# Performance work log

Measured on AMD Instinct MI355X. Metric: run time of the kernel, lower is better.

The kernel has to match this reference:

```python
import jax, jax.numpy as jnp
import numpy as np

TEMPERATURE = 0.07

def l2norm(x, eps=1e-12):
    # torch.nn.functional.normalize(dim=1): x / max(||x||, eps)
    n = jnp.sqrt(jnp.sum(x * x, axis=1, keepdims=True))
    return x / jnp.maximum(n, eps)

def setup_inputs() -> dict:
    key = jax.random.key(0)
    ks = jax.random.split(key, 8)
    B, D_in, H, M, Q, NNEG = 1024, 2048, 1024, 256, 65536, 16384
    return {
        "y1": jax.random.normal(ks[0], (B, D_in), dtype=jnp.float32),
        "y2": jax.random.normal(ks[1], (B, D_in), dtype=jnp.float32),
        "W_enc_q": jax.random.normal(ks[2], (D_in, H), dtype=jnp.float32) * 0.02,
        "W_enc_k": jax.random.normal(ks[3], (D_in, H), dtype=jnp.float32) * 0.02,
        "W_proj": jax.random.normal(ks[4], (H, M), dtype=jnp.float32) * 0.02,
        "queue": jax.random.normal(ks[5], (Q, M), dtype=jnp.float32),
        "sample_idx": jax.random.randint(ks[6], (NNEG,), 0, Q, dtype=jnp.int32),
        "write_idx": jnp.arange(B, dtype=jnp.int32),
    }

def reference(y1, y2, W_enc_q, W_enc_k, W_proj, queue, sample_idx, write_idx):
    # query path (trainable)
    q = l2norm((y2 @ W_enc_q) @ W_proj)                 # [B, M]
    # key path (no_grad in original)
    k = jax.lax.stop_gradient(l2norm((y1 @ W_enc_k) @ W_proj))  # [B, M]
    # sample negatives from GPU-resident queue (gather) + normalize
    neg = l2norm(queue[sample_idx])                     # [NNEG, M]
    pos_logits = jnp.sum(q * k, axis=1, keepdims=True)  # [B, 1]
    neg_logits = q @ neg.T                              # [B, NNEG]
    logits = jnp.concatenate([pos_logits, neg_logits], axis=1) / TEMPERATURE
    # cross_entropy with labels == 0
    loss = -jnp.mean(jax.nn.log_softmax(logits, axis=-1)[:, 0])
    # FIFO append modeled as circular-buffer scatter write
    new_queue = queue.at[write_idx].set(k)
    return loss, new_queue
```

## Files before the change

kernel.cpp:

```cpp
#include <hip/hip_runtime.h>
#include <hip/hip_bf16.h>
#include <math.h>
#include <stdint.h>


typedef __attribute__((ext_vector_type(4))) float floatx4;
typedef __attribute__((ext_vector_type(8))) short bf16x8;
typedef __attribute__((ext_vector_type(8))) unsigned short ushort8;

__device__ __forceinline__ unsigned short f2bf(float x) {
    union { float f; unsigned int u; } v; v.f = x;
    unsigned int r = v.u + 0x7FFFu + ((v.u >> 16) & 1u);
    return (unsigned short)(r >> 16);
}

__device__ __forceinline__ void async_cp16(const void* g, void* l) {
    auto gp = reinterpret_cast<const __attribute__((address_space(1))) unsigned int*>(
        reinterpret_cast<uintptr_t>(g));
    auto lp = reinterpret_cast<__attribute__((address_space(3))) unsigned int*>(
        reinterpret_cast<uintptr_t>(l));
    __builtin_amdgcn_global_load_lds(gp, lp, 16, 0, 0);
}

__global__ __launch_bounds__(256) void prep_all(
    const float* __restrict__ y2, const float* __restrict__ y1,
    const float* __restrict__ Wq, const float* __restrict__ Wk,
    const float* __restrict__ Wp,
    unsigned short* __restrict__ y2b, unsigned short* __restrict__ y1b,
    unsigned short* __restrict__ Wqb, unsigned short* __restrict__ Wkb,
    unsigned short* __restrict__ Wpt,
    int D, int H, int M) {
    __shared__ unsigned short tile[32][33];
    const int b = blockIdx.x, t = threadIdx.x;

    if (b < 4096) {
        const int g = b >> 10, i = b & 1023;
        const float* in = (g == 0) ? y2 : (g == 1) ? y1 : (g == 2) ? Wq : Wk;
        unsigned short* outp = (g == 0) ? y2b : (g == 1) ? y1b : (g == 2) ? Wqb : Wkb;
        long idx = (long)i * 256 + t;
        const float4* in4 = (const float4*)in;
        float4 a = in4[idx * 2], c = in4[idx * 2 + 1];
        ushort8 o;
        o[0] = f2bf(a.x); o[1] = f2bf(a.y); o[2] = f2bf(a.z); o[3] = f2bf(a.w);
        o[4] = f2bf(c.x); o[5] = f2bf(c.y); o[6] = f2bf(c.z); o[7] = f2bf(c.w);
        ((ushort8*)outp)[idx] = o;
        return;
    }
    int idx = b - 4096;
    const int R = H, C = M;
    int cb = C / 32;
    int c0 = (idx % cb) * 32, r0 = (idx / cb) * 32;
    int tx = t & 31, ty = t >> 5;
#pragma unroll
    for (int i = 0; i < 4; ++i)
        tile[ty + i * 8][tx] = f2bf(Wp[(size_t)(r0 + ty + i * 8) * C + c0 + tx]);
    __syncthreads();
#pragma unroll
    for (int i = 0; i < 4; ++i)
        Wpt[(size_t)(c0 + ty + i * 8) * R + r0 + tx] = tile[tx][ty + i * 8];
}

__global__ __launch_bounds__(256) void wc_plus(
    const unsigned short* __restrict__ Wpt,
    const unsigned short* __restrict__ Wqkb,
    unsigned short* __restrict__ Wct,
    const float* __restrict__ queue, const int* __restrict__ sidx,
    unsigned short* __restrict__ negb) {
    __shared__ unsigned short As[3][128 * 32];
    __shared__ unsigned short Bs[3][64 * 32];
    const int b = blockIdx.x, t = threadIdx.x;
    const int type = b % 3, id = b / 3;

    if (type == 0) {
        const int batch = id >> 6, rem = id & 63;
        const int row0 = (rem >> 5) * 128;
        const int col0 = (rem & 31) * 64;
        const unsigned short* A = Wpt;
        const unsigned short* Bp = Wqkb + (long)batch * 2048 * 1024;
        unsigned short* C = Wct + (long)batch * 256 * 2048;
        const int Ko = 1024, No = 2048, nIt = 32;
        const int lane = t & 63, wave = t >> 6;
        const int wr = wave >> 1, wc = wave & 1;
        const int lrow = lane & 15, quad = lane >> 4;

        floatx4 acc[4][2] = {};

        auto stage = [&](int kk, int p) {
            int c0 = t, c1 = t + 256;
            async_cp16(A + (size_t)(row0 + (c0 >> 2)) * Ko + kk + (c0 & 3) * 8,
                       (char*)(As[p]) + (size_t)c0 * 16);
            async_cp16(A + (size_t)(row0 + (c1 >> 2)) * Ko + kk + (c1 & 3) * 8,
                       (char*)(As[p]) + (size_t)c1 * 16);
            async_cp16(Bp + (size_t)(col0 + (t >> 2)) * Ko + kk + (t & 3) * 8,
                       (char*)(Bs[p]) + (size_t)t * 16);
        };
        auto compute = [&](int p) {
            bf16x8 af[4], bfr[2];
#pragma unroll
            for (int i = 0; i < 4; ++i)
                af[i] = *(const bf16x8*)(As[p] + (size_t)(wr * 64 + i * 16 + lrow) * 32 + quad * 8);
#pragma unroll
            for (int j = 0; j < 2; ++j)
                bfr[j] = *(const bf16x8*)(Bs[p] + (size_t)(wc * 32 + j * 16 + lrow) * 32 + quad * 8);
            __builtin_amdgcn_s_setprio(1);
#pragma unroll
            for (int i = 0; i < 4; ++i)
#pragma unroll
                for (int j = 0; j < 2; ++j)
                    acc[i][j] = __builtin_amdgcn_mfma_f32_16x16x32_bf16(af[i], bfr[j], acc[i][j], 0, 0, 0);
            __builtin_amdgcn_s_setprio(0);
        };

        stage(0, 0);
        stage(32, 1);
        for (int k = 0; k < nIt; ++k) {
            if (k + 2 < nIt) {
                stage((k + 2) * 32, (k + 2) % 3);
                asm volatile("s_waitcnt vmcnt(6)" ::: "memory");
            } else if (k + 2 == nIt) {
                asm volatile("s_waitcnt vmcnt(3)" ::: "memory");
            } else {
                asm volatile("s_waitcnt vmcnt(0)" ::: "memory");
            }
            __builtin_amdgcn_s_barrier();
            compute(k % 3);
            __builtin_amdgcn_s_barrier();
        }
#pragma unroll
        for (int i = 0; i < 4; ++i) {
            int grow = row0 + wr * 64 + i * 16 + quad * 4;
#pragma unroll
            for (int j = 0; j < 2; ++j) {
                int gcol = col0 + wc * 32 + j * 16 + lrow;
#pragma unroll
                for (int r = 0; r < 4; ++r)
                    C[(size_t)(grow + r) * No + gcol] = f2bf(acc[i][j][r]);
            }
        }
    } else {
        const int gid = id * 2 + (type == 2);
        const int w = t >> 6, lane = t & 63;
#pragma unroll
        for (int j = 0; j < 16; ++j) {
            int r = gid * 64 + w * 16 + j;
            const float4* src = (const float4*)(queue + (size_t)sidx[r] * 256);
            float4 v = src[lane];
            float ss = v.x * v.x + v.y * v.y + v.z * v.z + v.w * v.w;
#pragma unroll
            for (int off = 1; off < 64; off <<= 1) ss += __shfl_xor(ss, off);
            float inv = 1.f / fmaxf(sqrtf(ss), 1e-12f);
            unsigned short o[4] = { f2bf(v.x * inv), f2bf(v.y * inv),
                                    f2bf(v.z * inv), f2bf(v.w * inv) };
            *(unsigned long long*)(negb + (size_t)r * 256 + lane * 4) =
                *(unsigned long long*)o;
        }
    }
}

__global__ __launch_bounds__(256) void qk_plus(
    const unsigned short* __restrict__ Yb,
    const unsigned short* __restrict__ Wct,
    float* __restrict__ Pg,
    const float4* __restrict__ queue4, float4* __restrict__ newq4) {
    __shared__ unsigned short As[3][128 * 32];
    __shared__ unsigned short Bs[3][64 * 32];
    const int b = blockIdx.x, t = threadIdx.x;
    const int type = b % 3, id = b / 3;

    if (type == 0) {
        const int z = id >> 5, rem = id & 31;
        const int batch = z >> 2, split = z & 3;
        const int row0 = (rem >> 2) * 128;
        const int col0 = (rem & 3) * 64;
        const unsigned short* A = Yb + (long)batch * 1024 * 2048;
        const unsigned short* Bp = Wct + (long)batch * 256 * 2048;
        float* P = Pg + (long)z * 1024 * 256;
        const int Ko = 2048, No = 256, nIt = 16;
        const int kbeg = split * 512;
        const int lane = t & 63, wave = t >> 6;
        const int wr = wave >> 1, wc = wave & 1;
        const int lrow = lane & 15, quad = lane >> 4;

        floatx4 acc[4][2] = {};

        auto stage = [&](int kk, int p) {
            int c0 = t, c1 = t + 256;
            async_cp16(A + (size_t)(row0 + (c0 >> 2)) * Ko + kk + (c0 & 3) * 8,
                       (char*)(As[p]) + (size_t)c0 * 16);
            async_cp16(A + (size_t)(row0 + (c1 >> 2)) * Ko + kk + (c1 & 3) * 8,
                       (char*)(As[p]) + (size_t)c1 * 16);
            async_cp16(Bp + (size_t)(col0 + (t >> 2)) * Ko + kk + (t & 3) * 8,
                       (char*)(Bs[p]) + (size_t)t * 16);
        };
        auto compute = [&](int p) {
            bf16x8 af[4], bfr[2];
#pragma unroll
            for (int i = 0; i < 4; ++i)
                af[i] = *(const bf16x8*)(As[p] + (size_t)(wr * 64 + i * 16 + lrow) * 32 + quad * 8);
#pragma unroll
            for (int j = 0; j < 2; ++j)
                bfr[j] = *(const bf16x8*)(Bs[p] + (size_t)(wc * 32 + j * 16 + lrow) * 32 + quad * 8);
            __builtin_amdgcn_s_setprio(1);
#pragma unroll
            for (int i = 0; i < 4; ++i)
#pragma unroll
                for (int j = 0; j < 2; ++j)
                    acc[i][j] = __builtin_amdgcn_mfma_f32_16x16x32_bf16(af[i], bfr[j], acc[i][j], 0, 0, 0);
            __builtin_amdgcn_s_setprio(0);
        };

        stage(kbeg, 0);
        stage(kbeg + 32, 1);
        for (int k = 0; k < nIt; ++k) {
            if (k + 2 < nIt) {
                stage(kbeg + (k + 2) * 32, (k + 2) % 3);
                asm volatile("s_waitcnt vmcnt(6)" ::: "memory");
            } else if (k + 2 == nIt) {
                asm volatile("s_waitcnt vmcnt(3)" ::: "memory");
            } else {
                asm volatile("s_waitcnt vmcnt(0)" ::: "memory");
            }
            __builtin_amdgcn_s_barrier();
            compute(k % 3);
            __builtin_amdgcn_s_barrier();
        }
#pragma unroll
        for (int i = 0; i < 4; ++i) {
            int grow = row0 + wr * 64 + i * 16 + quad * 4;
#pragma unroll
            for (int j = 0; j < 2; ++j) {
                int gcol = col0 + wc * 32 + j * 16 + lrow;
#pragma unroll
                for (int r = 0; r < 4; ++r)
                    P[(size_t)(grow + r) * No + gcol] = acc[i][j][r];
            }
        }
    } else {
        const int cid = id * 2 + (type == 2);
        long base = (long)cid * 8192 + t;
#pragma unroll
        for (int o = 0; o < 4; ++o) {
            float4 v[8];
#pragma unroll
            for (int i = 0; i < 8; ++i) v[i] = queue4[base + (size_t)(o * 8 + i) * 256];
#pragma unroll
            for (int i = 0; i < 8; ++i) newq4[base + (size_t)(o * 8 + i) * 256] = v[i];
        }
    }
}

__global__ __launch_bounds__(256) void qk_finalize(const float* __restrict__ P,
                                                   const int* __restrict__ widx,
                                                   unsigned short* __restrict__ qkb,
                                                   float* __restrict__ newq,
                                                   float* __restrict__ pos,
                                                   float* __restrict__ sumexp,
                                                   int B_, int nsplit, float invT) {
    const int i = blockIdx.x, t = threadIdx.x;
    const long RM = (long)B_ * 256;
    float sq = 0.f, sk = 0.f;
    for (int s = 0; s < nsplit; ++s) {
        sq += P[(long)s * RM + (long)i * 256 + t];
        sk += P[(long)(nsplit + s) * RM + (long)i * 256 + t];
    }
    __shared__ float r0[256], r1[256], r2[256];
    r0[t] = sq * sq; r1[t] = sk * sk; r2[t] = sq * sk;
    __syncthreads();
    for (int off = 128; off > 0; off >>= 1) {
        if (t < off) { r0[t] += r0[t + off]; r1[t] += r1[t + off]; r2[t] += r2[t + off]; }
        __syncthreads();
    }
    float nq = fmaxf(sqrtf(r0[0]), 1e-12f);
    float nk = fmaxf(sqrtf(r1[0]), 1e-12f);
    float qn = sq / nq, kn = sk / nk;
    qkb[(size_t)i * 256 + t] = f2bf(qn);
    qkb[(size_t)(B_ + i) * 256 + t] = f2bf(kn);
    newq[(size_t)widx[i] * 256 + t] = kn;
    if (t == 0) {
        float p = (r2[0] / (nq * nk)) * invT;
        pos[i] = p;
        sumexp[i] = __expf(p);
    }
}

__global__ __launch_bounds__(256) void gemm_logits(const unsigned short* __restrict__ A,
                                                   const unsigned short* __restrict__ B,
                                                   float* __restrict__ sumexp,
                                                   int Ko, float invT) {
    __shared__ unsigned short As[128 * 64];
    __shared__ unsigned short Bs[128 * 64];
    __shared__ float rowred[128];
    const int row0 = blockIdx.y * 128, col0 = blockIdx.x * 128;
    const int t = threadIdx.x;
    const int lane = t & 63, wave = t >> 6;
    const int wr = wave >> 1, wc = wave & 1;
    const int lrow = lane & 15, quad = lane >> 4;

    floatx4 acc[4][4] = {};

    for (int kk = 0; kk < Ko; kk += 64) {
#pragma unroll
        for (int r = 0; r < 4; ++r) {
            int c = t + r * 256;
            async_cp16(A + (size_t)(row0 + (c >> 3)) * Ko + kk + (c & 7) * 8,
                       (char*)As + (size_t)c * 16);
            async_cp16(B + (size_t)(col0 + (c >> 3)) * Ko + kk + (c & 7) * 8,
                       (char*)Bs + (size_t)c * 16);
        }
        __syncthreads();
        bf16x8 af[4][2], bf[4][2];
#pragma unroll
        for (int i = 0; i < 4; ++i)
#pragma unroll
            for (int k2 = 0; k2 < 2; ++k2) {
                af[i][k2] = *(const bf16x8*)(As + (size_t)(wr * 64 + i * 16 + lrow) * 64 + k2 * 32 + quad * 8);
                bf[i][k2] = *(const bf16x8*)(Bs + (size_t)(wc * 64 + i * 16 + lrow) * 64 + k2 * 32 + quad * 8);
            }
#pragma unroll
        for (int k2 = 0; k2 < 2; ++k2)
#pragma unroll
            for (int i = 0; i < 4; ++i)
#pragma unroll
                for (int j = 0; j < 4; ++j)
                    acc[i][j] = __builtin_amdgcn_mfma_f32_16x16x32_bf16(af[i][k2], bf[j][k2], acc[i][j], 0, 0, 0);
        __syncthreads();
    }
    if (t < 128) rowred[t] = 0.f;
    __syncthreads();
#pragma unroll
    for (int i = 0; i < 4; ++i) {
#pragma unroll
        for (int r = 0; r < 4; ++r) {
            float s = 0.f;
#pragma unroll
            for (int j = 0; j < 4; ++j) s += __expf(acc[i][j][r] * invT);
            s += __shfl_xor(s, 1); s += __shfl_xor(s, 2);
            s += __shfl_xor(s, 4); s += __shfl_xor(s, 8);
            if (lrow == 0) atomicAdd(&rowred[wr * 64 + i * 16 + quad * 4 + r], s);
        }
    }
    __syncthreads();
    if (t < 128) atomicAdd(&sumexp[row0 + t], rowred[t]);
}

__global__ __launch_bounds__(256) void final_loss(const float* __restrict__ pos,
                                                  const float* __restrict__ sumexp,
                                                  float* __restrict__ out, int B_) {
    const int t = threadIdx.x;
    float acc = 0.f;
    for (int i = t; i < B_; i += 256) acc += logf(sumexp[i]) - pos[i];
    __shared__ float s[256];
    s[t] = acc;
    __syncthreads();
    for (int off = 128; off > 0; off >>= 1) {
        if (t < off) s[t] += s[t + off];
        __syncthreads();
    }
    if (t == 0) out[0] = s[0] / (float)B_;
}

extern "C" void kernel_launch(void* const* d_in, const int* in_sizes, int n_in,
                              void* d_out, int out_size, void* d_ws, size_t ws_size,
                              hipStream_t stream) {
    const float* y1    = (const float*)d_in[0];
    const float* y2    = (const float*)d_in[1];
    const float* Wq    = (const float*)d_in[2];
    const float* Wk    = (const float*)d_in[3];
    const float* Wp    = (const float*)d_in[4];
    const float* queue = (const float*)d_in[5];
    const int*   sidx  = (const int*)d_in[6];
    const int*   widx  = (const int*)d_in[7];
    float* out = (float*)d_out;

    const int B    = in_sizes[7];
    const int NNEG = in_sizes[6];
    const int D    = in_sizes[0] / B;
    const int H    = in_sizes[2] / D;
    const int M    = in_sizes[4] / H;
    const float invT = 1.0f / 0.07f;
    const int NS_P = 4;

    float* ws  = (float*)d_ws;
    float* Pp     = ws;
    float* pos    = Pp + (size_t)2 * NS_P * B * M;
    float* sumexp = pos + B;
    unsigned short* us = (unsigned short*)(sumexp + B);
    unsigned short* y2b  = us;
    unsigned short* y1b  = y2b + (size_t)B * D;
    unsigned short* Wqb  = y1b + (size_t)B * D;
    unsigned short* Wkb  = Wqb + (size_t)D * H;
    unsigned short* Wpt  = Wkb + (size_t)D * H;
    unsigned short* Wct  = Wpt + (size_t)M * H;
    unsigned short* qkb  = Wct + (size_t)2 * M * D;
    unsigned short* negb = qkb + (size_t)2 * B * M;

    const int nPrep = 4 * 1024 + (H / 32) * (M / 32);
    prep_all<<<nPrep, 256, 0, stream>>>(y2, y1, Wq, Wk, Wp,
                                        y2b, y1b, Wqb, Wkb, Wpt, D, H, M);

    wc_plus<<<384, 256, 0, stream>>>(Wpt, Wqb, Wct, queue, sidx, negb);

    qk_plus<<<768, 256, 0, stream>>>(y2b, Wct, Pp,
                                     (const float4*)queue, (float4*)(out + 1));

    qk_finalize<<<B, 256, 0, stream>>>(Pp, widx, qkb, out + 1, pos, sumexp,
                                       B, NS_P, invT);

    gemm_logits<<<dim3(NNEG / 128, B / 128), 256, 0, stream>>>(
        qkb, negb, sumexp, M, invT);

    final_loss<<<1, 256, 0, stream>>>(pos, sumexp, out, B);
}
```

Before: 216.6 us.

## Rebalance work across kernels and fuse final loss into logits GEMM

The negative-sample gather and normalize moves from wc_plus into prep_all, and the queue copy moves from qk_plus into wc_plus. The qk GEMM becomes a standalone kernel with 64-row tiles, giving 512 blocks instead of 256 GEMM blocks. The final_loss launch is removed: the last gemm_logits block to finish, found through an atomic counter that qk_finalize resets, computes the mean loss. This cuts one launch and rebalances co-scheduled work between stages, at the cost of a threadfence and atomic per block plus smaller GEMM tiles with less reuse.

```diff
diff --git a/kernel.cpp b/kernel.cpp
--- a/kernel.cpp
+++ b/kernel.cpp
@@ -29,6 +29,8 @@
     unsigned short* __restrict__ y2b, unsigned short* __restrict__ y1b,
     unsigned short* __restrict__ Wqb, unsigned short* __restrict__ Wkb,
     unsigned short* __restrict__ Wpt,
+    const float* __restrict__ queue, const int* __restrict__ sidx,
+    unsigned short* __restrict__ negb,
     int D, int H, int M) {
     __shared__ unsigned short tile[32][33];
     const int b = blockIdx.x, t = threadIdx.x;
@@ -46,30 +48,48 @@
         ((ushort8*)outp)[idx] = o;
         return;
     }
-    int idx = b - 4096;
-    const int R = H, C = M;
-    int cb = C / 32;
-    int c0 = (idx % cb) * 32, r0 = (idx / cb) * 32;
-    int tx = t & 31, ty = t >> 5;
-#pragma unroll
-    for (int i = 0; i < 4; ++i)
-        tile[ty + i * 8][tx] = f2bf(Wp[(size_t)(r0 + ty + i * 8) * C + c0 + tx]);
-    __syncthreads();
-#pragma unroll
-    for (int i = 0; i < 4; ++i)
-        Wpt[(size_t)(c0 + ty + i * 8) * R + r0 + tx] = tile[tx][ty + i * 8];
+    if (b < 4352) {
+        int idx = b - 4096;
+        const int R = H, C = M;
+        int cb = C / 32;
+        int c0 = (idx % cb) * 32, r0 = (idx / cb) * 32;
+        int tx = t & 31, ty = t >> 5;
+#pragma unroll
+        for (int i = 0; i < 4; ++i)
+            tile[ty + i * 8][tx] = f2bf(Wp[(size_t)(r0 + ty + i * 8) * C + c0 + tx]);
+        __syncthreads();
+#pragma unroll
+        for (int i = 0; i < 4; ++i)
+            Wpt[(size_t)(c0 + ty + i * 8) * R + r0 + tx] = tile[tx][ty + i * 8];
+        return;
+    }
+    const int gid = b - 4352;
+    const int w = t >> 6, lane = t & 63;
+#pragma unroll
+    for (int j = 0; j < 16; ++j) {
+        int r = gid * 64 + w * 16 + j;
+        const float4* src = (const float4*)(queue + (size_t)sidx[r] * 256);
+        float4 v = src[lane];
+        float ss = v.x * v.x + v.y * v.y + v.z * v.z + v.w * v.w;
+#pragma unroll
+        for (int off = 1; off < 64; off <<= 1) ss += __shfl_xor(ss, off);
+        float inv = 1.f / fmaxf(sqrtf(ss), 1e-12f);
+        unsigned short o[4] = { f2bf(v.x * inv), f2bf(v.y * inv),
+                                f2bf(v.z * inv), f2bf(v.w * inv) };
+        *(unsigned long long*)(negb + (size_t)r * 256 + lane * 4) =
+            *(unsigned long long*)o;
+    }
 }
 
 __global__ __launch_bounds__(256) void wc_plus(
     const unsigned short* __restrict__ Wpt,
     const unsigned short* __restrict__ Wqkb,
     unsigned short* __restrict__ Wct,
-    const float* __restrict__ queue, const int* __restrict__ sidx,
-    unsigned short* __restrict__ negb) {
+    const float4* __restrict__ queue4, float4* __restrict__ newq4) {
     __shared__ unsigned short As[3][128 * 32];
     __shared__ unsigned short Bs[3][64 * 32];
     const int b = blockIdx.x, t = threadIdx.x;
-    const int type = b % 3, id = b / 3;
+    const int type = b % 5, id = b / 5;
 
     if (type == 0) {
         const int batch = id >> 6, rem = id & 63;
@@ -138,113 +158,88 @@
             }
         }
     } else {
-        const int gid = id * 2 + (type == 2);
-        const int w = t >> 6, lane = t & 63;
-#pragma unroll
-        for (int j = 0; j < 16; ++j) {
-            int r = gid * 64 + w * 16 + j;
-            const float4* src = (const float4*)(queue + (size_t)sidx[r] * 256);
-            float4 v = src[lane];
-            float ss = v.x * v.x + v.y * v.y + v.z * v.z + v.w * v.w;
-#pragma unroll
-            for (int off = 1; off < 64; off <<= 1) ss += __shfl_xor(ss, off);
-            float inv = 1.f / fmaxf(sqrtf(ss), 1e-12f);
-            unsigned short o[4] = { f2bf(v.x * inv), f2bf(v.y * inv),
-                                    f2bf(v.z * inv), f2bf(v.w * inv) };
-            *(unsigned long long*)(negb + (size_t)r * 256 + lane * 4) =
-                *(unsigned long long*)o;
-        }
-    }
-}
-
-__global__ __launch_bounds__(256) void qk_plus(
+        const int cid = id * 4 + (type - 1);
+        long base = (long)cid * 8192 + t;
+#pragma unroll
+        for (int o = 0; o < 4; ++o) {
+            float4 v[8];
+#pragma unroll
+            for (int i = 0; i < 8; ++i) v[i] = queue4[base + (size_t)(o * 8 + i) * 256];
+#pragma unroll
+            for (int i = 0; i < 8; ++i) newq4[base + (size_t)(o * 8 + i) * 256] = v[i];
+        }
+    }
+}
+
+__global__ __launch_bounds__(256) void qk_gemm(
     const unsigned short* __restrict__ Yb,
     const unsigned short* __restrict__ Wct,
-    float* __restrict__ Pg,
-    const float4* __restrict__ queue4, float4* __restrict__ newq4) {
-    __shared__ unsigned short As[3][128 * 32];
+    float* __restrict__ Pg) {
+    __shared__ unsigned short As[3][64 * 32];
     __shared__ unsigned short Bs[3][64 * 32];
-    const int b = blockIdx.x, t = threadIdx.x;
-    const int type = b % 3, id = b / 3;
-
-    if (type == 0) {
-        const int z = id >> 5, rem = id & 31;
-        const int batch = z >> 2, split = z & 3;
-        const int row0 = (rem >> 2) * 128;
-        const int col0 = (rem & 3) * 64;
-        const unsigned short* A = Yb + (long)batch * 1024 * 2048;
-        const unsigned short* Bp = Wct + (long)batch * 256 * 2048;
-        float* P = Pg + (long)z * 1024 * 256;
-        const int Ko = 2048, No = 256, nIt = 16;
-        const int kbeg = split * 512;
-        const int lane = t & 63, wave = t >> 6;
-        const int wr = wave >> 1, wc = wave & 1;
-        const int lrow = lane & 15, quad = lane >> 4;
-
-        floatx4 acc[4][2] = {};
-
-        auto stage = [&](int kk, int p) {
-            int c0 = t, c1 = t + 256;
-            async_cp16(A + (size_t)(row0 + (c0 >> 2)) * Ko + kk + (c0 & 3) * 8,
-                       (char*)(As[p]) + (size_t)c0 * 16);
-            async_cp16(A + (size_t)(row0 + (c1 >> 2)) * Ko + kk + (c1 & 3) * 8,
-                       (char*)(As[p]) + (size_t)c1 * 16);
-            async_cp16(Bp + (size_t)(col0 + (t >> 2)) * Ko + kk + (t & 3) * 8,
-                       (char*)(Bs[p]) + (size_t)t * 16);
-        };
-        auto compute = [&](int p) {
-            bf16x8 af[4], bfr[2];
-#pragma unroll
-            for (int i = 0; i < 4; ++i)
-                af[i] = *(const bf16x8*)(As[p] + (size_t)(wr * 64 + i * 16 + lrow) * 32 + quad * 8);
+    const int id = blockIdx.x, t = threadIdx.x;
+    const int z = id >> 6, rem = id & 63;
+    const int batch = z >> 2, split = z & 3;
+    const int row0 = (rem >> 2) * 64;
+    const int col0 = (rem & 3) * 64;
+    const unsigned short* A = Yb + (long)batch * 1024 * 2048;
+    const unsigned short* Bp = Wct + (long)batch * 256 * 2048;
+    float* P = Pg + (long)z * 1024 * 256;
+    const int Ko = 2048, No = 256, nIt = 16;
+    const int kbeg = split * 512;
+    const int lane = t & 63, wave = t >> 6;
+    const int wr = wave >> 1, wc = wave & 1;
+    const int lrow = lane & 15, quad = lane >> 4;
+
+    floatx4 acc[2][2] = {};
+
+    auto stage = [&](int kk, int p) {
+        async_cp16(A + (size_t)(row0 + (t >> 2)) * Ko + kk + (t & 3) * 8,
+                   (char*)(As[p]) + (size_t)t * 16);
+        async_cp16(Bp + (size_t)(col0 + (t >> 2)) * Ko + kk + (t & 3) * 8,
+                   (char*)(Bs[p]) + (size_t)t * 16);
+    };
+    auto compute = [&](int p) {
+        bf16x8 af[2], bfr[2];
+#pragma unroll
+        for (int i = 0; i < 2; ++i)
+            af[i] = *(const bf16x8*)(As[p] + (size_t)(wr * 32 + i * 16 + lrow) * 32 + quad * 8);
+#pragma unroll
+        for (int j = 0; j < 2; ++j)
+            bfr[j] = *(const bf16x8*)(Bs[p] + (size_t)(wc * 32 + j * 16 + lrow) * 32 + quad * 8);
+        __builtin_amdgcn_s_setprio(1);
+#pragma unroll
+        for (int i = 0; i < 2; ++i)
 #pragma unroll
             for (int j = 0; j < 2; ++j)
-                bfr[j] = *(const bf16x8*)(Bs[p] + (size_t)(wc * 32 + j * 16 + lrow) * 32 + quad * 8);
-            __builtin_amdgcn_s_setprio(1);
-#pragma unroll
-            for (int i = 0; i < 4; ++i)
-#pragma unroll
-                for (int j = 0; j < 2; ++j)
-                    acc[i][j] = __builtin_amdgcn_mfma_f32_16x16x32_bf16(af[i], bfr[j], acc[i][j], 0, 0, 0);
-            __builtin_amdgcn_s_setprio(0);
-        };
-
-        stage(kbeg, 0);
-        stage(kbeg + 32, 1);
-        for (int k = 0; k < nIt; ++k) {
-            if (k + 2 < nIt) {
-                stage(kbeg + (k + 2) * 32, (k + 2) % 3);
-                asm volatile("s_waitcnt vmcnt(6)" ::: "memory");
-            } else if (k + 2 == nIt) {
-                asm volatile("s_waitcnt vmcnt(3)" ::: "memory");
-            } else {
-                asm volatile("s_waitcnt vmcnt(0)" ::: "memory");
-            }
-            __builtin_amdgcn_s_barrier();
-            compute(k % 3);
-            __builtin_amdgcn_s_barrier();
-        }
-#pragma unroll
-        for (int i = 0; i < 4; ++i) {
-            int grow = row0 + wr * 64 + i * 16 + quad * 4;
-#pragma unroll
-            for (int j = 0; j < 2; ++j) {
-                int gcol = col0 + wc * 32 + j * 16 + lrow;
-#pragma unroll
-                for (int r = 0; r < 4; ++r)
-                    P[(size_t)(grow + r) * No + gcol] = acc[i][j][r];
-            }
-        }
-    } else {
-        const int cid = id * 2 + (type == 2);
-        long base = (long)cid * 8192 + t;
-#pragma unroll
-        for (int o = 0; o < 4; ++o) {
-            float4 v[8];
-#pragma unroll
-            for (int i = 0; i < 8; ++i) v[i] = queue4[base + (size_t)(o * 8 + i) * 256];
-#pragma unroll
-            for (int i = 0; i < 8; ++i) newq4[base + (size_t)(o * 8 + i) * 256] = v[i];
+                acc[i][j] = __builtin_amdgcn_mfma_f32_16x16x32_bf16(af[i], bfr[j], acc[i][j], 0, 0, 0);
+        __builtin_amdgcn_s_setprio(0);
+    };
+
+    stage(kbeg, 0);
+    stage(kbeg + 32, 1);
+    for (int k = 0; k < nIt; ++k) {
+        if (k + 2 < nIt) {
+            stage(kbeg + (k + 2) * 32, (k + 2) % 3);
+            asm volatile("s_waitcnt vmcnt(4)" ::: "memory");
+        } else if (k + 2 == nIt) {
+            asm volatile("s_waitcnt vmcnt(2)" ::: "memory");
+        } else {
+            asm volatile("s_waitcnt vmcnt(0)" ::: "memory");
+        }
+        __builtin_amdgcn_s_barrier();
+        compute(k % 3);
+        __builtin_amdgcn_s_barrier();
+    }
+#pragma unroll
+    for (int i = 0; i < 2; ++i) {
+        int grow = row0 + wr * 32 + i * 16 + quad * 4;
+#pragma unroll
+        for (int j = 0; j < 2; ++j) {
+            int gcol = col0 + wc * 32 + j * 16 + lrow;
+#pragma unroll
+            for (int r = 0; r < 4; ++r)
+                P[(size_t)(grow + r) * No + gcol] = acc[i][j][r];
         }
     }
 }
@@ -255,8 +250,10 @@
                                                    float* __restrict__ newq,
                                                    float* __restrict__ pos,
                                                    float* __restrict__ sumexp,
+                                                   unsigned int* __restrict__ ctr,
                                                    int B_, int nsplit, float invT) {
     const int i = blockIdx.x, t = threadIdx.x;
+    if (i == 0 && t == 0) *ctr = 0u;
     const long RM = (long)B_ * 256;
     float sq = 0.f, sk = 0.f;
     for (int s = 0; s < nsplit; ++s) {
@@ -286,7 +283,11 @@
 __global__ __launch_bounds__(256) void gemm_logits(const unsigned short* __restrict__ A,
                                                    const unsigned short* __restrict__ B,
                                                    float* __restrict__ sumexp,
-                                                   int Ko, float invT) {
+                                                   const float* __restrict__ pos,
+                                                   float* __restrict__ out,
+                                                   unsigned int* __restrict__ ctr,
+                                                   int Ko, int B_, int nblocks,
+                                                   float invT) {
     __shared__ unsigned short As[128 * 64];
     __shared__ unsigned short Bs[128 * 64];
     __shared__ float rowred[128];
@@ -341,22 +342,25 @@
     }
     __syncthreads();
     if (t < 128) atomicAdd(&sumexp[row0 + t], rowred[t]);
-}
-
-__global__ __launch_bounds__(256) void final_loss(const float* __restrict__ pos,
-                                                  const float* __restrict__ sumexp,
-                                                  float* __restrict__ out, int B_) {
-    const int t = threadIdx.x;
-    float acc = 0.f;
-    for (int i = t; i < B_; i += 256) acc += logf(sumexp[i]) - pos[i];
-    __shared__ float s[256];
-    s[t] = acc;
+
+    __threadfence();
     __syncthreads();
-    for (int off = 128; off > 0; off >>= 1) {
-        if (t < off) s[t] += s[t + off];
+    __shared__ int lastdone;
+    if (t == 0) lastdone = (atomicAdd(ctr, 1u) == (unsigned)(nblocks - 1));
+    __syncthreads();
+    if (lastdone) {
+        float accl = 0.f;
+        for (int i = t; i < B_; i += 256)
+            accl += logf(atomicAdd(&sumexp[i], 0.0f)) - pos[i];
+        __shared__ float sred[256];
+        sred[t] = accl;
         __syncthreads();
-    }
-    if (t == 0) out[0] = s[0] / (float)B_;
+        for (int off = 128; off > 0; off >>= 1) {
+            if (t < off) sred[t] += sred[t + off];
+            __syncthreads();
+        }
+        if (t == 0) out[0] = sred[0] / (float)B_;
+    }
 }
 
 extern "C" void kernel_launch(void* const* d_in, const int* in_sizes, int n_in,
@@ -384,7 +388,8 @@
     float* Pp     = ws;
     float* pos    = Pp + (size_t)2 * NS_P * B * M;
     float* sumexp = pos + B;
-    unsigned short* us = (unsigned short*)(sumexp + B);
+    unsigned int* ctr = (unsigned int*)(sumexp + B);
+    unsigned short* us = (unsigned short*)(ctr + 64);
     unsigned short* y2b  = us;
     unsigned short* y1b  = y2b + (size_t)B * D;
     unsigned short* Wqb  = y1b + (size_t)B * D;
@@ -394,20 +399,20 @@
     unsigned short* qkb  = Wct + (size_t)2 * M * D;
     unsigned short* negb = qkb + (size_t)2 * B * M;
 
-    const int nPrep = 4 * 1024 + (H / 32) * (M / 32);
+    const int nPrep = 4 * 1024 + (H / 32) * (M / 32) + NNEG / 64;
     prep_all<<<nPrep, 256, 0, stream>>>(y2, y1, Wq, Wk, Wp,
-                                        y2b, y1b, Wqb, Wkb, Wpt, D, H, M);
-
-    wc_plus<<<384, 256, 0, stream>>>(Wpt, Wqb, Wct, queue, sidx, negb);
-
-    qk_plus<<<768, 256, 0, stream>>>(y2b, Wct, Pp,
+                                        y2b, y1b, Wqb, Wkb, Wpt,
+                                        queue, sidx, negb, D, H, M);
+
+    wc_plus<<<640, 256, 0, stream>>>(Wpt, Wqb, Wct,
                                      (const float4*)queue, (float4*)(out + 1));
 
+    qk_gemm<<<512, 256, 0, stream>>>(y2b, Wct, Pp);
+
     qk_finalize<<<B, 256, 0, stream>>>(Pp, widx, qkb, out + 1, pos, sumexp,
-                                       B, NS_P, invT);
-
+                                       ctr, B, NS_P, invT);
+
+    const int nLog = (NNEG / 128) * (B / 128);
     gemm_logits<<<dim3(NNEG / 128, B / 128), 256, 0, stream>>>(
-        qkb, negb, sumexp, M, invT);
-
-    final_loss<<<1, 256, 0, stream>>>(pos, sumexp, out, B);
-}
+        qkb, negb, sumexp, pos, out, ctr, M, B, nLog, invT);
+}
```

Result: slower. 274.4 us (+26.7%).
